# Kernel tuning notes

Hardware: AMD Instinct MI355X
Metric: run time of the kernel (lower is better)

Reference implementation:

```python
import jax, jax.numpy as jnp
import numpy as np

B, TM1, N, H = 512, 256, 128, 64  # batch, T-1, input_size, hidden_size


def setup_inputs() -> dict:
    key = jax.random.key(0)
    ks = jax.random.split(key, 7)
    s = 0.05
    return {
        "input_data": jax.random.normal(ks[0], (B, TM1, N), dtype=jnp.float32),
        "attn_w": jax.random.normal(ks[1], (1, 2 * H + TM1), dtype=jnp.float32) * s,
        "attn_b": jax.random.normal(ks[2], (1,), dtype=jnp.float32) * s,
        "W_ih": jax.random.normal(ks[3], (4 * H, N), dtype=jnp.float32) * s,
        "W_hh": jax.random.normal(ks[4], (4 * H, H), dtype=jnp.float32) * s,
        "b_ih": jax.random.normal(ks[5], (4 * H,), dtype=jnp.float32) * s,
        "b_hh": jax.random.normal(ks[6], (4 * H,), dtype=jnp.float32) * s,
    }


def reference(input_data, attn_w, attn_b, W_ih, W_hh, b_ih, b_hh):
    b, tm1, n = input_data.shape
    h_dim = W_hh.shape[1]
    # (B, N, T-1): each driving series over the full window, used every step
    x_series = jnp.transpose(input_data, (0, 2, 1))
    aw = attn_w[0]  # (2H + T-1,)
    ab = attn_b[0]

    def step(carry, x_t):  # x_t: (B, N) inputs at time t
        h, c = carry  # (B, H) each
        # attention scores: concat(h, c, x_series) @ aw, done without materializing concat
        s_hc = h @ aw[:h_dim] + c @ aw[h_dim:2 * h_dim]  # (B,)
        s_x = x_series @ aw[2 * h_dim:]  # (B, N)
        a = jax.nn.softmax(s_x + s_hc[:, None] + ab, axis=1)  # softmax over driving series
        wx = a * x_t  # (B, N) weighted input
        # single LSTM cell step (PyTorch gate order i, f, g, o)
        gates = wx @ W_ih.T + b_ih + h @ W_hh.T + b_hh  # (B, 4H)
        i, f, g, o = jnp.split(gates, 4, axis=1)
        c2 = jax.nn.sigmoid(f) * c + jax.nn.sigmoid(i) * jnp.tanh(g)
        h2 = jax.nn.sigmoid(o) * jnp.tanh(c2)
        return (h2, c2), (wx, h2)

    h0 = jnp.zeros((b, h_dim), dtype=input_data.dtype)
    c0 = jnp.zeros((b, h_dim), dtype=input_data.dtype)
    xs = jnp.transpose(input_data, (1, 0, 2))  # (T-1, B, N)
    _, (wxs, hs) = jax.lax.scan(step, (h0, c0), xs)
    input_weighted = jnp.transpose(wxs, (1, 0, 2))  # (B, T-1, N)
    input_encoded = jnp.transpose(hs, (1, 0, 2))  # (B, T-1, H)
    return input_weighted, input_encoded
```

## Files before the change

kernel.cpp:

```cpp
#include <hip/hip_runtime.h>
#include <hip/hip_fp16.h>
#include <cstdint>
#include <cstddef>

#define B_ 512
#define T_ 256
#define N_ 128
#define H_ 64
#define G_ 256

typedef __attribute__((ext_vector_type(8))) short short8;
typedef __attribute__((ext_vector_type(4))) float f32x4;
typedef _Float16 half2_t __attribute__((ext_vector_type(2)));

static __device__ __forceinline__ unsigned short f2bf(float f) {
    union { float f; unsigned int i; } v;
    v.f = f;
    unsigned int x = v.i;
    return (unsigned short)((x + 0x7fffu + ((x >> 16) & 1u)) >> 16);
}
static __device__ __forceinline__ half2_t u2h2(unsigned int u) {
    union { unsigned int u; half2_t h; } v; v.u = u; return v.h;
}

__global__ __launch_bounds__(256) void k_wpack(const float* __restrict__ W_hh,
                                               uint4* __restrict__ wpack) {
    int idx = blockIdx.x * 256 + threadIdx.x;
    if (idx >= 2048) return;
    int g = idx >> 9, q = (idx >> 6) & 7, j = idx & 63;
    const float* src = W_hh + ((size_t)(g * H_ + j)) * H_ + q * 8;
    float4 a = *(const float4*)(src);
    float4 b = *(const float4*)(src + 4);
    union { uint4 u; half2_t h[4]; } pk;
    pk.h[0] = (half2_t){(_Float16)a.x, (_Float16)a.y};
    pk.h[1] = (half2_t){(_Float16)a.z, (_Float16)a.w};
    pk.h[2] = (half2_t){(_Float16)b.x, (_Float16)b.y};
    pk.h[3] = (half2_t){(_Float16)b.z, (_Float16)b.w};
    wpack[idx] = pk.u;
}

__global__ __launch_bounds__(256) void k_awgemm(const float* __restrict__ x,
                                                const float* __restrict__ attn_w,
                                                const float* __restrict__ W_ih,
                                                const float* __restrict__ b_ih,
                                                const float* __restrict__ b_hh,
                                                float* __restrict__ iw,
                                                _Float16* __restrict__ gatesx) {
    __shared__ __align__(16) unsigned short Wl[G_][136];
    __shared__ __align__(16) unsigned short Al[32][136];
    __shared__ float bias[G_];
    __shared__ float aw_s[T_];
    __shared__ float a_s[N_];
    __shared__ float wred[4];
    const int tid = threadIdx.x;
    const int b = blockIdx.x;

    for (int q = tid; q < G_ * 32; q += 256) {
        int r = q >> 5, c4 = (q & 31) << 2;
        float4 v = *(const float4*)(W_ih + r * N_ + c4);
        Wl[r][c4 + 0] = f2bf(v.x); Wl[r][c4 + 1] = f2bf(v.y);
        Wl[r][c4 + 2] = f2bf(v.z); Wl[r][c4 + 3] = f2bf(v.w);
    }
    bias[tid] = b_ih[tid] + b_hh[tid];
    aw_s[tid] = attn_w[2 * H_ + tid];
    __syncthreads();

    float (*red)[128] = (float(*)[128])&Al[0][0];
    const int n0 = (tid & 31) << 2;
    const int tg = tid >> 5;
    const float* xb = x + (size_t)b * (T_ * N_);
    {
        float p0 = 0.f, p1 = 0.f, p2 = 0.f, p3 = 0.f;
        for (int t = tg; t < T_; t += 8) {
            float4 v = *(const float4*)(xb + t * N_ + n0);
            float w = aw_s[t];
            p0 += v.x * w; p1 += v.y * w; p2 += v.z * w; p3 += v.w * w;
        }
        red[tg][n0 + 0] = p0; red[tg][n0 + 1] = p1;
        red[tg][n0 + 2] = p2; red[tg][n0 + 3] = p3;
    }
    __syncthreads();
    {
        float s = 0.f;
        if (tid < 128) {
            #pragma unroll
            for (int g = 0; g < 8; ++g) s += red[g][tid];
        }
        float m = (tid < 128) ? s : -1e30f;
        #pragma unroll
        for (int d = 1; d < 64; d <<= 1) m = fmaxf(m, __shfl_xor(m, d));
        if ((tid & 63) == 0) wred[tid >> 6] = m;
        __syncthreads();
        m = fmaxf(wred[0], wred[1]);
        __syncthreads();
        float e = (tid < 128) ? __expf(s - m) : 0.f;
        float z = e;
        #pragma unroll
        for (int d = 1; d < 64; d <<= 1) z += __shfl_xor(z, d);
        if ((tid & 63) == 0) wred[tid >> 6] = z;
        __syncthreads();
        z = wred[0] + wred[1];
        if (tid < 128) a_s[tid] = e / z;
    }
    __syncthreads();

    const int lane = tid & 63;
    const int lr = lane & 15;
    const int lk = (lane >> 4) << 3;
    const int gc0 = (tid >> 6) << 6;
    const int orow = (lane >> 4) << 2;

    for (int st = 0; st < 8; ++st) {
        const int r0 = b * T_ + st * 32;
        __syncthreads();
        for (int q = tid; q < 32 * 32; q += 256) {
            int r = q >> 5, c4 = (q & 31) << 2;
            size_t off = (size_t)(r0 + r) * N_ + c4;
            float4 v = *(const float4*)(x + off);
            float4 w;
            w.x = a_s[c4 + 0] * v.x; w.y = a_s[c4 + 1] * v.y;
            w.z = a_s[c4 + 2] * v.z; w.w = a_s[c4 + 3] * v.w;
            *(float4*)(iw + off) = w;
            Al[r][c4 + 0] = f2bf(w.x); Al[r][c4 + 1] = f2bf(w.y);
            Al[r][c4 + 2] = f2bf(w.z); Al[r][c4 + 3] = f2bf(w.w);
        }
        __syncthreads();

        f32x4 acc[2][4];
        #pragma unroll
        for (int mt = 0; mt < 2; ++mt)
            #pragma unroll
            for (int nt = 0; nt < 4; ++nt)
                acc[mt][nt] = (f32x4){0.f, 0.f, 0.f, 0.f};

        #pragma unroll
        for (int kk = 0; kk < N_; kk += 32) {
            short8 af0 = *(const short8*)(&Al[lr][kk + lk]);
            short8 af1 = *(const short8*)(&Al[16 + lr][kk + lk]);
            #pragma unroll
            for (int nt = 0; nt < 4; ++nt) {
                short8 bfv = *(const short8*)(&Wl[gc0 + nt * 16 + lr][kk + lk]);
                acc[0][nt] = __builtin_amdgcn_mfma_f32_16x16x32_bf16(af0, bfv, acc[0][nt], 0, 0, 0);
                acc[1][nt] = __builtin_amdgcn_mfma_f32_16x16x32_bf16(af1, bfv, acc[1][nt], 0, 0, 0);
            }
        }
        #pragma unroll
        for (int mt = 0; mt < 2; ++mt) {
            #pragma unroll
            for (int nt = 0; nt < 4; ++nt) {
                int col = gc0 + nt * 16 + lr;
                float bs = bias[col];
                int cell = col & 63, qg = col >> 6;
                #pragma unroll
                for (int rg = 0; rg < 4; ++rg) {
                    int rr = r0 + mt * 16 + orow + rg;
                    gatesx[((size_t)rr * H_ + cell) * 4 + qg] =
                        (_Float16)(acc[mt][nt][rg] + bs);
                }
            }
        }
    }
}

__global__ __attribute__((amdgpu_flat_work_group_size(64, 64)))
__attribute__((amdgpu_waves_per_eu(1, 1)))
void k_rnn10(const _Float16* __restrict__ gatesx,
             const uint4* __restrict__ wpack,
             float* __restrict__ enc) {
    __shared__ __align__(16) _Float16 hs[H_];
    const int j = threadIdx.x;
    const int b = blockIdx.x;

    uint4 wv[4][8];
    #pragma unroll
    for (int g = 0; g < 4; ++g) {
        #pragma unroll
        for (int q = 0; q < 8; ++q) {
            unsigned voff = (unsigned)((((g << 3) + q) * 64 + j) << 4);
            asm volatile("global_load_dwordx4 %0, %1, %2"
                         : "=v"(wv[g][q]) : "v"(voff), "s"(wpack) : "memory");
        }
    }
    asm volatile("s_waitcnt vmcnt(0)" ::: "memory");

    hs[j] = (_Float16)0.f;
    float c = 0.f;

    const _Float16* gx = gatesx + ((size_t)b * T_ * H_ + j) * 4;
    float* ep = enc + (size_t)b * T_ * H_ + j;

    uint2 gA = *(const uint2*)(gx);
    uint2 gB = *(const uint2*)(gx + G_);

#define STEP(GREG, TNEXT)                                                   \
    {                                                                       \
        half2_t gif = u2h2(GREG.x), ggo = u2h2(GREG.y);                     \
        float a0 = (float)gif.x, a1 = (float)gif.y;                         \
        float a2 = (float)ggo.x, a3 = (float)ggo.y;                         \
        int tn_ = (TNEXT) < T_ ? (TNEXT) : (T_ - 1);                        \
        GREG = *(const uint2*)(gx + (size_t)tn_ * G_);                      \
        const uint4* hv4 = (const uint4*)hs;                                \
        _Pragma("unroll")                                                   \
        for (int q = 0; q < 8; ++q) {                                       \
            uint4 ch = hv4[q];               \
            a0 = __builtin_amdgcn_fdot2(u2h2(wv[0][q].x), u2h2(ch.x), a0, false); \
            a1 = __builtin_amdgcn_fdot2(u2h2(wv[1][q].x), u2h2(ch.x), a1, false); \
            a2 = __builtin_amdgcn_fdot2(u2h2(wv[2][q].x), u2h2(ch.x), a2, false); \
            a3 = __builtin_amdgcn_fdot2(u2h2(wv[3][q].x), u2h2(ch.x), a3, false); \
            a0 = __builtin_amdgcn_fdot2(u2h2(wv[0][q].y), u2h2(ch.y), a0, false); \
            a1 = __builtin_amdgcn_fdot2(u2h2(wv[1][q].y), u2h2(ch.y), a1, false); \
            a2 = __builtin_amdgcn_fdot2(u2h2(wv[2][q].y), u2h2(ch.y), a2, false); \
            a3 = __builtin_amdgcn_fdot2(u2h2(wv[3][q].y), u2h2(ch.y), a3, false); \
            a0 = __builtin_amdgcn_fdot2(u2h2(wv[0][q].z), u2h2(ch.z), a0, false); \
            a1 = __builtin_amdgcn_fdot2(u2h2(wv[1][q].z), u2h2(ch.z), a1, false); \
            a2 = __builtin_amdgcn_fdot2(u2h2(wv[2][q].z), u2h2(ch.z), a2, false); \
            a3 = __builtin_amdgcn_fdot2(u2h2(wv[3][q].z), u2h2(ch.z), a3, false); \
            a0 = __builtin_amdgcn_fdot2(u2h2(wv[0][q].w), u2h2(ch.w), a0, false); \
            a1 = __builtin_amdgcn_fdot2(u2h2(wv[1][q].w), u2h2(ch.w), a1, false); \
            a2 = __builtin_amdgcn_fdot2(u2h2(wv[2][q].w), u2h2(ch.w), a2, false); \
            a3 = __builtin_amdgcn_fdot2(u2h2(wv[3][q].w), u2h2(ch.w), a3, false); \
        }                                                                   \
        float si = 1.f / (1.f + __expf(-a0));                               \
        float sf = 1.f / (1.f + __expf(-a1));                               \
        float tg = 1.f - 2.f / (__expf(2.f * a2) + 1.f);                    \
        float so = 1.f / (1.f + __expf(-a3));                               \
        c = sf * c + si * tg;                                               \
        float tc = 1.f - 2.f / (__expf(2.f * c) + 1.f);                     \
        float h = so * tc;                                                  \
        hs[j] = (_Float16)h;         \
        *ep = h;                                                            \
        ep += H_;                                                           \
    }

    for (int t = 0; t < T_; t += 2) {
        STEP(gA, t + 2);
        STEP(gB, t + 3);
    }
#undef STEP
}

extern "C" void kernel_launch(void* const* d_in, const int* in_sizes, int n_in,
                              void* d_out, int out_size, void* d_ws, size_t ws_size,
                              hipStream_t stream) {
    if (n_in < 7 || in_sizes[0] != B_ * T_ * N_) return;

    const float* x    = (const float*)d_in[0];
    const float* aw   = (const float*)d_in[1];
    const float* W_ih = (const float*)d_in[3];
    const float* W_hh = (const float*)d_in[4];
    const float* b_ih = (const float*)d_in[5];
    const float* b_hh = (const float*)d_in[6];

    float* iwp = (float*)d_out;
    float* enc = (float*)d_out + (size_t)B_ * T_ * N_;

    size_t gx_bytes = (size_t)B_ * T_ * G_ * sizeof(_Float16);
    _Float16* gatesx = (_Float16*)d_ws;
    uint4* wpack = (uint4*)((char*)d_ws + gx_bytes);
    size_t need = gx_bytes + 2048 * sizeof(uint4);
    if (ws_size < need) return;

    hipLaunchKernelGGL(k_wpack, dim3(8), dim3(256), 0, stream, W_hh, wpack);
    hipLaunchKernelGGL(k_awgemm, dim3(B_), dim3(256), 0, stream,
                       x, aw, W_ih, b_ih, b_hh, iwp, gatesx);
    hipLaunchKernelGGL(k_rnn10, dim3(B_), dim3(64), 0, stream, gatesx, wpack, enc);
}
```

Measured before the change: 184.7 us.

## Stage input window once in LDS as bf16 and keep pre-packed W_ih in registers

The attention-GEMM kernel now writes the whole per-batch input window into shared memory as bf16 during the attention-score pass. It reuses that copy for the weighted-input output and the gate GEMM, instead of reading x from global memory a second time. A new small kernel pre-packs W_ih into MFMA fragment order, and each wave loads its fragments straight into registers, which removes the per-block LDS staging and conversion of W_ih. The trade-offs are a large LDS footprint, and a weighted-input output that is now computed from bf16-rounded x, which adds precision error to that output.

```diff
diff --git a/kernel.cpp b/kernel.cpp
--- a/kernel.cpp
+++ b/kernel.cpp
@@ -13,6 +13,11 @@
 typedef __attribute__((ext_vector_type(4))) float f32x4;
 typedef _Float16 half2_t __attribute__((ext_vector_type(2)));
 
+static __device__ __forceinline__ float bf2f(unsigned short u) {
+    union { unsigned int i; float f; } v;
+    v.i = ((unsigned int)u) << 16;
+    return v.f;
+}
 static __device__ __forceinline__ unsigned short f2bf(float f) {
     union { float f; unsigned int i; } v;
     v.f = f;
@@ -39,33 +44,58 @@
     wpack[idx] = pk.u;
 }
 
-__global__ __launch_bounds__(256) void k_awgemm(const float* __restrict__ x,
-                                                const float* __restrict__ attn_w,
-                                                const float* __restrict__ W_ih,
-                                                const float* __restrict__ b_ih,
-                                                const float* __restrict__ b_hh,
-                                                float* __restrict__ iw,
-                                                _Float16* __restrict__ gatesx) {
-    __shared__ __align__(16) unsigned short Wl[G_][136];
-    __shared__ __align__(16) unsigned short Al[32][136];
+__global__ __launch_bounds__(256) void k_wpackIH(const float* __restrict__ W_ih,
+                                                 uint4* __restrict__ wp) {
+    int idx = blockIdx.x * 256 + threadIdx.x;
+    if (idx >= 4096) return;
+    int lane = idx & 63;
+    int rest = idx >> 6;
+    int kc = rest & 3, nt = (rest >> 2) & 3, w = rest >> 4;
+    int row = w * 64 + nt * 16 + (lane & 15);
+    int kb  = kc * 32 + (lane >> 4) * 8;
+    const float* src = W_ih + (size_t)row * N_ + kb;
+    union { uint4 u; unsigned short s[8]; } pk;
+    #pragma unroll
+    for (int e = 0; e < 8; ++e) pk.s[e] = f2bf(src[e]);
+    wp[idx] = pk.u;
+}
+
+__global__ __attribute__((amdgpu_flat_work_group_size(256, 256)))
+__attribute__((amdgpu_waves_per_eu(2, 2)))
+void k_awgemm2(const float* __restrict__ x,
+               const float* __restrict__ attn_w,
+               const uint4* __restrict__ wih,
+               const float* __restrict__ b_ih,
+               const float* __restrict__ b_hh,
+               float* __restrict__ iw,
+               _Float16* __restrict__ gatesx) {
+    __shared__ __align__(16) unsigned short Xl[T_][136];
+    __shared__ float red2[8][128];
     __shared__ float bias[G_];
     __shared__ float aw_s[T_];
     __shared__ float a_s[N_];
     __shared__ float wred[4];
     const int tid = threadIdx.x;
     const int b = blockIdx.x;
-
-    for (int q = tid; q < G_ * 32; q += 256) {
-        int r = q >> 5, c4 = (q & 31) << 2;
-        float4 v = *(const float4*)(W_ih + r * N_ + c4);
-        Wl[r][c4 + 0] = f2bf(v.x); Wl[r][c4 + 1] = f2bf(v.y);
-        Wl[r][c4 + 2] = f2bf(v.z); Wl[r][c4 + 3] = f2bf(v.w);
-    }
+    const int lane = tid & 63;
+    const int w = tid >> 6;
+
+    uint4 bfw[4][4];
+    #pragma unroll
+    for (int nt = 0; nt < 4; ++nt) {
+        #pragma unroll
+        for (int kc = 0; kc < 4; ++kc) {
+            unsigned voff = (unsigned)((((w * 4 + nt) * 4 + kc) * 64 + lane) << 4);
+            asm volatile("global_load_dwordx4 %0, %1, %2"
+                         : "=v"(bfw[nt][kc]) : "v"(voff), "s"(wih) : "memory");
+        }
+    }
+    asm volatile("s_waitcnt vmcnt(0)" ::: "memory");
+
     bias[tid] = b_ih[tid] + b_hh[tid];
     aw_s[tid] = attn_w[2 * H_ + tid];
     __syncthreads();
 
-    float (*red)[128] = (float(*)[128])&Al[0][0];
     const int n0 = (tid & 31) << 2;
     const int tg = tid >> 5;
     const float* xb = x + (size_t)b * (T_ * N_);
@@ -73,18 +103,20 @@
         float p0 = 0.f, p1 = 0.f, p2 = 0.f, p3 = 0.f;
         for (int t = tg; t < T_; t += 8) {
             float4 v = *(const float4*)(xb + t * N_ + n0);
-            float w = aw_s[t];
-            p0 += v.x * w; p1 += v.y * w; p2 += v.z * w; p3 += v.w * w;
-        }
-        red[tg][n0 + 0] = p0; red[tg][n0 + 1] = p1;
-        red[tg][n0 + 2] = p2; red[tg][n0 + 3] = p3;
+            float wt = aw_s[t];
+            p0 += v.x * wt; p1 += v.y * wt; p2 += v.z * wt; p3 += v.w * wt;
+            Xl[t][n0 + 0] = f2bf(v.x); Xl[t][n0 + 1] = f2bf(v.y);
+            Xl[t][n0 + 2] = f2bf(v.z); Xl[t][n0 + 3] = f2bf(v.w);
+        }
+        red2[tg][n0 + 0] = p0; red2[tg][n0 + 1] = p1;
+        red2[tg][n0 + 2] = p2; red2[tg][n0 + 3] = p3;
     }
     __syncthreads();
     {
         float s = 0.f;
         if (tid < 128) {
             #pragma unroll
-            for (int g = 0; g < 8; ++g) s += red[g][tid];
+            for (int g = 0; g < 8; ++g) s += red2[g][tid];
         }
         float m = (tid < 128) ? s : -1e30f;
         #pragma unroll
@@ -104,25 +136,23 @@
     }
     __syncthreads();
 
-    const int lane = tid & 63;
     const int lr = lane & 15;
     const int lk = (lane >> 4) << 3;
-    const int gc0 = (tid >> 6) << 6;
+    const int gc0 = w << 6;
     const int orow = (lane >> 4) << 2;
 
     for (int st = 0; st < 8; ++st) {
-        const int r0 = b * T_ + st * 32;
-        __syncthreads();
+        const int r0g = b * T_ + st * 32;
         for (int q = tid; q < 32 * 32; q += 256) {
             int r = q >> 5, c4 = (q & 31) << 2;
-            size_t off = (size_t)(r0 + r) * N_ + c4;
-            float4 v = *(const float4*)(x + off);
-            float4 w;
-            w.x = a_s[c4 + 0] * v.x; w.y = a_s[c4 + 1] * v.y;
-            w.z = a_s[c4 + 2] * v.z; w.w = a_s[c4 + 3] * v.w;
-            *(float4*)(iw + off) = w;
-            Al[r][c4 + 0] = f2bf(w.x); Al[r][c4 + 1] = f2bf(w.y);
-            Al[r][c4 + 2] = f2bf(w.z); Al[r][c4 + 3] = f2bf(w.w);
+            int row = st * 32 + r;
+            ushort4 xv = *(const ushort4*)(&Xl[row][c4]);
+            float4 wv4;
+            wv4.x = a_s[c4 + 0] * bf2f(xv.x); wv4.y = a_s[c4 + 1] * bf2f(xv.y);
+            wv4.z = a_s[c4 + 2] * bf2f(xv.z); wv4.w = a_s[c4 + 3] * bf2f(xv.w);
+            *(float4*)(iw + (size_t)(r0g + r) * N_ + c4) = wv4;
+            Xl[row][c4 + 0] = f2bf(wv4.x); Xl[row][c4 + 1] = f2bf(wv4.y);
+            Xl[row][c4 + 2] = f2bf(wv4.z); Xl[row][c4 + 3] = f2bf(wv4.w);
         }
         __syncthreads();
 
@@ -134,12 +164,12 @@
                 acc[mt][nt] = (f32x4){0.f, 0.f, 0.f, 0.f};
 
         #pragma unroll
-        for (int kk = 0; kk < N_; kk += 32) {
-            short8 af0 = *(const short8*)(&Al[lr][kk + lk]);
-            short8 af1 = *(const short8*)(&Al[16 + lr][kk + lk]);
+        for (int kc = 0; kc < 4; ++kc) {
+            short8 af0 = *(const short8*)(&Xl[st * 32 + lr][kc * 32 + lk]);
+            short8 af1 = *(const short8*)(&Xl[st * 32 + 16 + lr][kc * 32 + lk]);
             #pragma unroll
             for (int nt = 0; nt < 4; ++nt) {
-                short8 bfv = *(const short8*)(&Wl[gc0 + nt * 16 + lr][kk + lk]);
+                short8 bfv = *(const short8*)(&bfw[nt][kc]);
                 acc[0][nt] = __builtin_amdgcn_mfma_f32_16x16x32_bf16(af0, bfv, acc[0][nt], 0, 0, 0);
                 acc[1][nt] = __builtin_amdgcn_mfma_f32_16x16x32_bf16(af1, bfv, acc[1][nt], 0, 0, 0);
             }
@@ -153,7 +183,7 @@
                 int cell = col & 63, qg = col >> 6;
                 #pragma unroll
                 for (int rg = 0; rg < 4; ++rg) {
-                    int rr = r0 + mt * 16 + orow + rg;
+                    int rr = r0g + mt * 16 + orow + rg;
                     gatesx[((size_t)rr * H_ + cell) * 4 + qg] =
                         (_Float16)(acc[mt][nt][rg] + bs);
                 }
@@ -257,11 +287,14 @@
     size_t gx_bytes = (size_t)B_ * T_ * G_ * sizeof(_Float16);
     _Float16* gatesx = (_Float16*)d_ws;
     uint4* wpack = (uint4*)((char*)d_ws + gx_bytes);
-    size_t need = gx_bytes + 2048 * sizeof(uint4);
+    uint4* wih   = wpack + 2048;
+    size_t need = gx_bytes + 2048 * sizeof(uint4) + 4096 * sizeof(uint4);
     if (ws_size < need) return;
 
     hipLaunchKernelGGL(k_wpack, dim3(8), dim3(256), 0, stream, W_hh, wpack);
-    hipLaunchKernelGGL(k_awgemm, dim3(B_), dim3(256), 0, stream,
-                       x, aw, W_ih, b_ih, b_hh, iwp, gatesx);
-    hipLaunchKernelGGL(k_rnn10, dim3(B_), dim3(64), 0, stream, gatesx, wpack, enc);
-}
+    hipLaunchKernelGGL(k_wpackIH, dim3(16), dim3(256), 0, stream, W_ih, wih);
+    hipLaunchKernelGGL(k_awgemm2, dim3(B_), dim3(256), 0, stream,
+                       x, aw, wih, b_ih, b_hh, iwp, gatesx);
+    hipLaunchKernelGGL(k_rnn10, dim3(B_), dim3(64), 0, stream,
+                       gatesx, wpack, enc);
+}
```

New measurement: 177.6 us. 3.8% less time.
